# Optimization experiments

Hardware: AMD Instinct MI355X
Metric: run time of the kernel (lower is better)

The kernel has to match this reference:

```python
import jax, jax.numpy as jnp
import numpy as np

NEG_INF = -1e9

def setup_inputs() -> dict:
    key = jax.random.key(0)
    ks = jax.random.split(key, 8)
    B, Np1, D, k = 16, 10001, 128, 16
    return {
        "query": jax.random.normal(ks[0], (B, D), jnp.float32),
        "psi_prime": jax.random.normal(ks[1], (B, Np1, D), jnp.float32),
        "knn_indices": jax.random.randint(ks[2], (B, Np1, k), 0, Np1, jnp.int64),
        "mask": jnp.zeros((B, Np1), dtype=bool),
        "current_coords": jax.random.uniform(ks[3], (B, 2), jnp.float32),
        "all_coords": jax.random.uniform(ks[4], (B, Np1, 2), jnp.float32),
        "demands": jax.random.uniform(ks[5], (B, Np1), jnp.float32),
        "lambda_param": jnp.float32(0.1),
        "mu_param": jnp.float32(0.5),
        "nu_param": jnp.float32(0.0),
    }

def _eknn(psi_prime, knn_indices):
    # psi_prime: [B, N+1, D], knn_indices: [B, N+1, k] -> interference [B, N+1]
    B, Np1, k = knn_indices.shape
    D = psi_prime.shape[-1]
    flat_idx = knn_indices.reshape(B, Np1 * k, 1)  # gather along node axis
    neighbors = jnp.take_along_axis(psi_prime, flat_idx, axis=1).reshape(B, Np1, k, D)
    return jnp.einsum("bnd,bnkd->bn", psi_prime, neighbors)

def reference(query, psi_prime, knn_indices, mask, current_coords, all_coords,
              demands, lambda_param, mu_param, nu_param):
    capacity = 1.0  # default forward arg
    context_scores = jnp.einsum("bnd,bd->bn", psi_prime, query)
    interference = _eknn(psi_prime, knn_indices)
    dist_to_nodes = jnp.linalg.norm(all_coords - current_coords[:, None, :], axis=-1)
    mu_eff = jnp.clip(mu_param, 0.0, 20.0)
    lam_eff = jnp.clip(lambda_param, -2.0, 3.0)
    nu_eff = jnp.clip(nu_param, -2.0, 3.0)
    scores = context_scores + lam_eff * interference - mu_eff * dist_to_nodes
    cap_val = max(float(capacity), 1e-8)
    scores = scores + nu_eff * (demands / cap_val)
    scores = jnp.where(mask, NEG_INF, scores)
    return jax.nn.log_softmax(scores, axis=-1)
```

## Files before the change

### kernel.cpp

```cpp
#include <hip/hip_runtime.h>
#include <math.h>

#define BATCH 16
#define NP1   10001
#define KNN   16
#define DIM   128
#define NEG_INF_F (-1e9f)
#define TOTAL_NODES ((long)BATCH * NP1)
#define SLAB_BYTES  ((size_t)BATCH * NP1 * DIM)
#define NXCD 8
#define EXP_OFF 60.0f
#define NBUCK 64

template <int SEL>
__device__ inline float f8tof(unsigned u) {
#if __has_builtin(__builtin_amdgcn_cvt_f32_fp8)
    return __builtin_amdgcn_cvt_f32_fp8((int)u, SEL);
#else
    const unsigned x = (u >> (8 * SEL)) & 0xFFu;
    const unsigned bits = ((x & 0x80u) << 24) | (((x & 0x7Fu) << 20) + 0x3C000000u);
    return (x & 0x7Fu) ? __uint_as_float(bits) : 0.f;
#endif
}

#if !__has_builtin(__builtin_amdgcn_cvt_pk_fp8_f32)
__device__ inline unsigned enc1_fp8(float f) {
    const unsigned u = __float_as_uint(f);
    const unsigned s = (u >> 31) << 7;
    unsigned v = u + 0x80000u;
    int e8 = (int)((v >> 23) & 0xFFu) - 120;
    if (e8 <= 0) return s;
    if (e8 > 15) { e8 = 15; v |= 0x700000u; }
    return s | ((unsigned)e8 << 3) | ((v >> 20) & 7u);
}
#endif

__device__ inline unsigned pk_fp8x4(float4 v) {
#if __has_builtin(__builtin_amdgcn_cvt_pk_fp8_f32)
    int w = __builtin_amdgcn_cvt_pk_fp8_f32(v.x, v.y, 0, false);
    w = __builtin_amdgcn_cvt_pk_fp8_f32(v.z, v.w, w, true);
    return (unsigned)w;
#else
    return enc1_fp8(v.x) | (enc1_fp8(v.y) << 8) | (enc1_fp8(v.z) << 16) | (enc1_fp8(v.w) << 24);
#endif
}

__device__ inline unsigned xcd_chunk_swizzle(unsigned b, unsigned nwg) {
    const unsigned xcd = b % NXCD, i = b / NXCD;
    const unsigned q = nwg / NXCD, r = nwg % NXCD;
    const unsigned base = (xcd < r) ? xcd * (q + 1) : r * (q + 1) + (xcd - r) * q;
    return base + i;
}

__global__ __launch_bounds__(256) void hs_prep_kernel(
    const float* __restrict__ query,
    const float* __restrict__ psi,
    const float* __restrict__ cur,
    const float* __restrict__ coords,
    const float* __restrict__ demands,
    const float* __restrict__ mu_p,
    const float* __restrict__ nu_p,
    unsigned* __restrict__ slab,
    float* __restrict__ out,
    float* __restrict__ bucket)
{
    if (blockIdx.x == 0) {
#pragma unroll
        for (int i = 0; i < (BATCH * NBUCK) / 256; ++i)
            bucket[threadIdx.x + i * 256] = 0.f;
    }

    const unsigned lb = xcd_chunk_swizzle(blockIdx.x, gridDim.x);
    const long row = (long)lb * 8 + (threadIdx.x >> 5);
    if (row >= TOTAL_NODES) return;
    const int l32 = threadIdx.x & 31;
    const int b = (int)(row / NP1);

    const float4 v = ((const float4*)psi)[row * 32 + l32];
    const float4 q = ((const float4*)query)[(long)b * 32 + l32];

    slab[row * 32 + l32] = pk_fp8x4(v);

    float ctx = v.x * q.x + v.y * q.y + v.z * q.z + v.w * q.w;
#pragma unroll
    for (int off = 16; off > 0; off >>= 1) ctx += __shfl_xor(ctx, off, 64);

    if (l32 == 0) {
        const float mu = fminf(fmaxf(mu_p[0], 0.f), 20.f);
        const float nu = fminf(fmaxf(nu_p[0], -2.f), 3.f);
        const float dx = coords[row * 2 + 0] - cur[b * 2 + 0];
        const float dy = coords[row * 2 + 1] - cur[b * 2 + 1];
        out[row] = ctx - mu * sqrtf(dx * dx + dy * dy) + nu * demands[row];
    }
}

__global__ __launch_bounds__(256) void hs_gather_kernel(
    const int* __restrict__ knn,
    const unsigned char* __restrict__ mask,
    const uint2* __restrict__ slab2,
    const float* __restrict__ lam_p,
    float* __restrict__ out,
    float* __restrict__ bucket)
{
    __shared__ float s_val[16];
    __shared__ int   s_bat[16];

    const unsigned lb = xcd_chunk_swizzle(blockIdx.x, gridDim.x);
    const int wid  = threadIdx.x >> 6;
    const int lane = threadIdx.x & 63;
    const int qw   = lane >> 4;
    const int l16  = lane & 15;
    const long node = ((long)lb * 4 + wid) * 4 + qw;
    const int b = (int)(node / NP1);
    const uint2* gb = slab2 + (long)b * NP1 * 16;

    float base = 0.f; int mk = 0;
    if (l16 == 0) { base = out[node]; mk = mask[node]; }

    const uint2 p = slab2[node * 16 + l16];
    const float pf0 = f8tof<0>(p.x), pf1 = f8tof<1>(p.x), pf2 = f8tof<2>(p.x), pf3 = f8tof<3>(p.x);
    const float pf4 = f8tof<0>(p.y), pf5 = f8tof<1>(p.y), pf6 = f8tof<2>(p.y), pf7 = f8tof<3>(p.y);

    const int4* kp = (const int4*)(knn + node * KNN);
    const int4 k0 = kp[0], k1 = kp[1], k2 = kp[2], k3 = kp[3];

    uint2 nb[KNN];
    nb[ 0] = gb[(long)k0.x * 16 + l16];
    nb[ 1] = gb[(long)k0.y * 16 + l16];
    nb[ 2] = gb[(long)k0.z * 16 + l16];
    nb[ 3] = gb[(long)k0.w * 16 + l16];
    nb[ 4] = gb[(long)k1.x * 16 + l16];
    nb[ 5] = gb[(long)k1.y * 16 + l16];
    nb[ 6] = gb[(long)k1.z * 16 + l16];
    nb[ 7] = gb[(long)k1.w * 16 + l16];
    nb[ 8] = gb[(long)k2.x * 16 + l16];
    nb[ 9] = gb[(long)k2.y * 16 + l16];
    nb[10] = gb[(long)k2.z * 16 + l16];
    nb[11] = gb[(long)k2.w * 16 + l16];
    nb[12] = gb[(long)k3.x * 16 + l16];
    nb[13] = gb[(long)k3.y * 16 + l16];
    nb[14] = gb[(long)k3.z * 16 + l16];
    nb[15] = gb[(long)k3.w * 16 + l16];

    float a0 = 0.f, a1 = 0.f, a2 = 0.f, a3 = 0.f;
    float a4 = 0.f, a5 = 0.f, a6 = 0.f, a7 = 0.f;
#pragma unroll
    for (int t = 0; t < KNN; ++t) {
        a0 = fmaf(f8tof<0>(nb[t].x), pf0, a0);
        a1 = fmaf(f8tof<1>(nb[t].x), pf1, a1);
        a2 = fmaf(f8tof<2>(nb[t].x), pf2, a2);
        a3 = fmaf(f8tof<3>(nb[t].x), pf3, a3);
        a4 = fmaf(f8tof<0>(nb[t].y), pf4, a4);
        a5 = fmaf(f8tof<1>(nb[t].y), pf5, a5);
        a6 = fmaf(f8tof<2>(nb[t].y), pf6, a6);
        a7 = fmaf(f8tof<3>(nb[t].y), pf7, a7);
    }
    float interf = ((a0 + a1) + (a2 + a3)) + ((a4 + a5) + (a6 + a7));

#pragma unroll
    for (int off = 8; off > 0; off >>= 1) interf += __shfl_xor(interf, off, 64);

    const int slot = wid * 4 + qw;
    if (l16 == 0) {
        const float lam = fminf(fmaxf(lam_p[0], -2.f), 3.f);
        float s = base + lam * interf;
        if (mk) s = NEG_INF_F;
        out[node] = s;
        s_val[slot] = expf(s - EXP_OFF);
        s_bat[slot] = b;
    }
    __syncthreads();

    if (threadIdx.x == 0) {
        float sum0 = 0.f, sum1 = 0.f;
        const int b0 = s_bat[0];
        int b1 = -1;
#pragma unroll
        for (int i = 0; i < 16; ++i) {
            if (s_bat[i] == b0) sum0 += s_val[i];
            else { b1 = s_bat[i]; sum1 += s_val[i]; }
        }
        const int bk = blockIdx.x & (NBUCK - 1);
        atomicAdd(&bucket[b0 * NBUCK + bk], sum0);
        if (b1 >= 0) atomicAdd(&bucket[b1 * NBUCK + bk], sum1);
    }
}

__global__ __launch_bounds__(256) void hs_finalize_kernel(
    float* __restrict__ out, const float* __restrict__ bucket)
{
    __shared__ float s_part[256];
    __shared__ float s_lse[BATCH];

    {
        const int t = threadIdx.x;
        const int bb = t >> 4, j = t & 15;
        s_part[t] = bucket[bb * NBUCK + j] + bucket[bb * NBUCK + j + 16]
                  + bucket[bb * NBUCK + j + 32] + bucket[bb * NBUCK + j + 48];
    }
    __syncthreads();
    if (threadIdx.x < BATCH) {
        float s = 0.f;
#pragma unroll
        for (int i = 0; i < 16; ++i) s += s_part[threadIdx.x * 16 + i];
        s_lse[threadIdx.x] = EXP_OFF + logf(s);
    }
    __syncthreads();

    const long t = (long)blockIdx.x * blockDim.x + threadIdx.x;
    const long n4 = TOTAL_NODES / 4;
    if (t >= n4) return;
    float4 v = ((float4*)out)[t];
    const long e0 = t * 4;
    v.x -= s_lse[(int)((e0    ) / NP1)];
    v.y -= s_lse[(int)((e0 + 1) / NP1)];
    v.z -= s_lse[(int)((e0 + 2) / NP1)];
    v.w -= s_lse[(int)((e0 + 3) / NP1)];
    ((float4*)out)[t] = v;
}

__global__ __launch_bounds__(256) void hs_scores_f32_kernel(
    const float* __restrict__ query, const float* __restrict__ psi,
    const int* __restrict__ knn, const unsigned char* __restrict__ mask,
    const float* __restrict__ cur, const float* __restrict__ coords,
    const float* __restrict__ demands, const float* __restrict__ lam_p,
    const float* __restrict__ mu_p, const float* __restrict__ nu_p,
    float* __restrict__ out)
{
    const int wid  = threadIdx.x >> 6;
    const int lane = threadIdx.x & 63;
    const int half = lane >> 5;
    const int l32  = lane & 31;
    const long node = (long)blockIdx.x * 4 + wid;
    if (node >= TOTAL_NODES) return;
    const int b = (int)(node / NP1);

    const float4* psi4 = (const float4*)psi;
    const float4* gb   = psi4 + (long)b * NP1 * 32;

    const float4 p = psi4[node * 32 + l32];
    const float4 q = ((const float4*)query)[(long)b * 32 + l32];
    float ctx = p.x * q.x + p.y * q.y + p.z * q.z + p.w * q.w;

    const int2* kp2 = (const int2*)(knn + node * KNN);
    int idxs[KNN / 2];
#pragma unroll
    for (int t = 0; t < KNN / 2; ++t) {
        const int2 pr = kp2[t];
        idxs[t] = half ? pr.y : pr.x;
    }
    float4 nb[KNN / 2];
#pragma unroll
    for (int t = 0; t < KNN / 2; ++t) nb[t] = gb[(long)idxs[t] * 32 + l32];

    float4 s0;
    s0.x = ((nb[0].x + nb[1].x) + (nb[2].x + nb[3].x)) + ((nb[4].x + nb[5].x) + (nb[6].x + nb[7].x));
    s0.y = ((nb[0].y + nb[1].y) + (nb[2].y + nb[3].y)) + ((nb[4].y + nb[5].y) + (nb[6].y + nb[7].y));
    s0.z = ((nb[0].z + nb[1].z) + (nb[2].z + nb[3].z)) + ((nb[4].z + nb[5].z) + (nb[6].z + nb[7].z));
    s0.w = ((nb[0].w + nb[1].w) + (nb[2].w + nb[3].w)) + ((nb[4].w + nb[5].w) + (nb[6].w + nb[7].w));
    float interf = p.x * s0.x + p.y * s0.y + p.z * s0.z + p.w * s0.w;

#pragma unroll
    for (int off = 32; off > 0; off >>= 1) {
        ctx    += __shfl_xor(ctx, off, 64);
        interf += __shfl_xor(interf, off, 64);
    }
    if (lane == 0) {
        const float lam = fminf(fmaxf(lam_p[0], -2.f), 3.f);
        const float mu  = fminf(fmaxf(mu_p[0],   0.f), 20.f);
        const float nu  = fminf(fmaxf(nu_p[0],  -2.f), 3.f);
        const float dx = coords[node * 2 + 0] - cur[b * 2 + 0];
        const float dy = coords[node * 2 + 1] - cur[b * 2 + 1];
        float s = 0.5f * ctx + lam * interf - mu * sqrtf(dx * dx + dy * dy) + nu * demands[node];
        if (mask[node]) s = NEG_INF_F;
        out[node] = s;
    }
}

#define LSM_T 1024
__global__ __launch_bounds__(LSM_T) void hs_lsm_kernel(float* __restrict__ out)
{
    const int b = blockIdx.x;
    float* row = out + (long)b * NP1;
    const int lane = threadIdx.x & 63;
    const int wid  = threadIdx.x >> 6;
    __shared__ float red[LSM_T / 64];

    float v[10];
    float mx = -INFINITY;
#pragma unroll
    for (int i = 0; i < 10; ++i) {
        const int idx = threadIdx.x + i * LSM_T;
        v[i] = (idx < NP1) ? row[idx] : -INFINITY;
        mx = fmaxf(mx, v[i]);
    }
#pragma unroll
    for (int off = 32; off > 0; off >>= 1) mx = fmaxf(mx, __shfl_xor(mx, off, 64));
    if (lane == 0) red[wid] = mx;
    __syncthreads();
    if (wid == 0) {
        float m = (lane < LSM_T / 64) ? red[lane] : -INFINITY;
#pragma unroll
        for (int off = 8; off > 0; off >>= 1) m = fmaxf(m, __shfl_xor(m, off, 64));
        if (lane == 0) red[0] = m;
    }
    __syncthreads();
    mx = red[0];
    __syncthreads();

    float sum = 0.f;
#pragma unroll
    for (int i = 0; i < 10; ++i) {
        const int idx = threadIdx.x + i * LSM_T;
        if (idx < NP1) sum += expf(v[i] - mx);
    }
#pragma unroll
    for (int off = 32; off > 0; off >>= 1) sum += __shfl_xor(sum, off, 64);
    if (lane == 0) red[wid] = sum;
    __syncthreads();
    if (wid == 0) {
        float s = (lane < LSM_T / 64) ? red[lane] : 0.f;
#pragma unroll
        for (int off = 8; off > 0; off >>= 1) s += __shfl_xor(s, off, 64);
        if (lane == 0) red[0] = s;
    }
    __syncthreads();
    const float lse = mx + logf(red[0]);
#pragma unroll
    for (int i = 0; i < 10; ++i) {
        const int idx = threadIdx.x + i * LSM_T;
        if (idx < NP1) row[idx] = v[i] - lse;
    }
}

extern "C" void kernel_launch(void* const* d_in, const int* in_sizes, int n_in,
                              void* d_out, int out_size, void* d_ws, size_t ws_size,
                              hipStream_t stream) {
    (void)in_sizes; (void)n_in; (void)out_size;

    const float* query   = (const float*)d_in[0];
    const float* psi     = (const float*)d_in[1];
    const int*   knn     = (const int*)d_in[2];
    const unsigned char* mask = (const unsigned char*)d_in[3];
    const float* cur     = (const float*)d_in[4];
    const float* coords  = (const float*)d_in[5];
    const float* demands = (const float*)d_in[6];
    const float* lam_p   = (const float*)d_in[7];
    const float* mu_p    = (const float*)d_in[8];
    const float* nu_p    = (const float*)d_in[9];
    float* out = (float*)d_out;

    const size_t bucket_bytes = (size_t)BATCH * NBUCK * sizeof(float);

    if (ws_size >= SLAB_BYTES + bucket_bytes) {
        unsigned* slab = (unsigned*)d_ws;
        float* bucket  = (float*)((char*)d_ws + SLAB_BYTES);

        const int prep_blocks = (int)((TOTAL_NODES + 7) / 8);
        hipLaunchKernelGGL(hs_prep_kernel, dim3(prep_blocks), dim3(256), 0, stream,
                           query, psi, cur, coords, demands, mu_p, nu_p, slab, out,
                           bucket);

        const int gat_blocks = (int)(TOTAL_NODES / 16);
        hipLaunchKernelGGL(hs_gather_kernel, dim3(gat_blocks), dim3(256), 0, stream,
                           knn, mask, (const uint2*)d_ws, lam_p, out, bucket);

        const int fin_blocks = (int)((TOTAL_NODES / 4 + 255) / 256);
        hipLaunchKernelGGL(hs_finalize_kernel, dim3(fin_blocks), dim3(256), 0, stream,
                           out, bucket);
    } else {
        const int blocks = (int)((TOTAL_NODES + 3) / 4);
        hipLaunchKernelGGL(hs_scores_f32_kernel, dim3(blocks), dim3(256), 0, stream,
                           query, psi, knn, mask, cur, coords, demands,
                           lam_p, mu_p, nu_p, out);
        hipLaunchKernelGGL(hs_lsm_kernel, dim3(BATCH), dim3(LSM_T), 0, stream, out);
    }
}
```

Measured before the change: 58.98 us.

## Fuse prep, gather and finalize into one cooperative producer/consumer kernel

Replaces the three-kernel chain with a single cooperative launch. 512 producer blocks quantize psi to fp8 and compute base scores batch by batch, then publish per-batch ready flags. 512 consumer blocks spin on those flags and run the kNN gather as soon as their batch is ready, and a grid sync precedes the log-softmax normalization. The aim is to overlap the prep and gather phases and remove launch gaps. In exchange it adds flag polling, a memset, per-launch host queries, a grid barrier, and a fixed grid that may underuse the device. The f32 fallback path is removed, so too small a workspace now produces no output.

```diff
diff --git a/kernel.cpp b/kernel.cpp
--- a/kernel.cpp
+++ b/kernel.cpp
@@ -1,5 +1,8 @@
 #include <hip/hip_runtime.h>
+#include <hip/hip_cooperative_groups.h>
 #include <math.h>
+
+namespace cg = cooperative_groups;
 
 #define BATCH 16
 #define NP1   10001
@@ -8,9 +11,15 @@
 #define NEG_INF_F (-1e9f)
 #define TOTAL_NODES ((long)BATCH * NP1)
 #define SLAB_BYTES  ((size_t)BATCH * NP1 * DIM)
-#define NXCD 8
 #define EXP_OFF 60.0f
 #define NBUCK 64
+
+#define PROD_BLOCKS 512
+#define CONS_BLOCKS 512
+#define FUSE_GRID   (PROD_BLOCKS + CONS_BLOCKS)
+#define NGRP_PREP   ((NP1 + 7) / 8)
+#define NGRP_GAT    ((int)(TOTAL_NODES / 16))
+#define FLAG_STRIDE 32
 
 template <int SEL>
 __device__ inline float f8tof(unsigned u) {
@@ -45,6 +54,7 @@
 #endif
 }
 
+#define NXCD 8
 __device__ inline unsigned xcd_chunk_swizzle(unsigned b, unsigned nwg) {
     const unsigned xcd = b % NXCD, i = b / NXCD;
     const unsigned q = nwg / NXCD, r = nwg % NXCD;
@@ -52,39 +62,200 @@
     return base + i;
 }
 
-__global__ __launch_bounds__(256) void hs_prep_kernel(
-    const float* __restrict__ query,
-    const float* __restrict__ psi,
-    const float* __restrict__ cur,
-    const float* __restrict__ coords,
-    const float* __restrict__ demands,
-    const float* __restrict__ mu_p,
-    const float* __restrict__ nu_p,
+__global__ __launch_bounds__(256, 4) void hs_fused_kernel(
+    const float* __restrict__ query, const float* __restrict__ psi,
+    const int* __restrict__ knn, const unsigned char* __restrict__ mask,
+    const float* __restrict__ cur, const float* __restrict__ coords,
+    const float* __restrict__ demands, const float* __restrict__ lam_p,
+    const float* __restrict__ mu_p, const float* __restrict__ nu_p,
     unsigned* __restrict__ slab,
     float* __restrict__ out,
-    float* __restrict__ bucket)
+    float* __restrict__ bucket,
+    unsigned* __restrict__ flags)
+{
+    __shared__ float s_val[16];
+    __shared__ int   s_bat[16];
+    __shared__ float s_part[256];
+    __shared__ float s_lse[BATCH];
+
+    const int tid = threadIdx.x;
+
+    if (blockIdx.x < PROD_BLOCKS) {
+        const int l32 = tid & 31;
+        const int hw  = tid >> 5;
+        const float mu = fminf(fmaxf(mu_p[0], 0.f), 20.f);
+        const float nuv = fminf(fmaxf(nu_p[0], -2.f), 3.f);
+        for (int b = 0; b < BATCH; ++b) {
+            const float4 q = ((const float4*)query)[b * 32 + l32];
+            const float cx = cur[2 * b], cy = cur[2 * b + 1];
+            const long rb = (long)b * NP1;
+            for (int g = blockIdx.x; g < NGRP_PREP; g += PROD_BLOCKS) {
+                const int r = g * 8 + hw;
+                if (r < NP1) {
+                    const long row = rb + r;
+                    const float4 v = ((const float4*)psi)[row * 32 + l32];
+                    slab[row * 32 + l32] = pk_fp8x4(v);
+                    float ctx = v.x * q.x + v.y * q.y + v.z * q.z + v.w * q.w;
+#pragma unroll
+                    for (int off = 16; off > 0; off >>= 1) ctx += __shfl_xor(ctx, off, 64);
+                    if (l32 == 0) {
+                        const float dx = coords[row * 2] - cx, dy = coords[row * 2 + 1] - cy;
+                        out[row] = ctx - mu * sqrtf(dx * dx + dy * dy) + nuv * demands[row];
+                    }
+                }
+            }
+            __threadfence();
+            __syncthreads();
+            if (tid == 0) atomicAdd(&flags[b * FLAG_STRIDE], 1u);
+        }
+    } else {
+        const int cblk = blockIdx.x - PROD_BLOCKS;
+        const int wid = tid >> 6, lane = tid & 63;
+        const int qw = lane >> 4, l16 = lane & 15;
+        const float lam = fminf(fmaxf(lam_p[0], -2.f), 3.f);
+        int b_ready = -1;
+        for (int vg = cblk; vg < NGRP_GAT; vg += CONS_BLOCKS) {
+            const long node0 = (long)vg * 16;
+            const int b_hi = (int)((node0 + 15) / NP1);
+            if (b_hi > b_ready) {
+                if (tid == 0) {
+                    while (__hip_atomic_load(&flags[b_hi * FLAG_STRIDE],
+                                             __ATOMIC_ACQUIRE, __HIP_MEMORY_SCOPE_AGENT)
+                           < (unsigned)PROD_BLOCKS)
+                        __builtin_amdgcn_s_sleep(16);
+                }
+                __syncthreads();
+                __threadfence();
+                b_ready = b_hi;
+            }
+            const long node = node0 + wid * 4 + qw;
+            const int b = (int)(node / NP1);
+            const uint2* gb = (const uint2*)slab + (long)b * NP1 * 16;
+
+            float base = 0.f; int mk = 0;
+            if (l16 == 0) { base = out[node]; mk = mask[node]; }
+
+            const uint2 p = ((const uint2*)slab)[node * 16 + l16];
+            const float pf0 = f8tof<0>(p.x), pf1 = f8tof<1>(p.x), pf2 = f8tof<2>(p.x), pf3 = f8tof<3>(p.x);
+            const float pf4 = f8tof<0>(p.y), pf5 = f8tof<1>(p.y), pf6 = f8tof<2>(p.y), pf7 = f8tof<3>(p.y);
+
+            const int4* kp = (const int4*)(knn + node * KNN);
+            const int4 k0 = kp[0], k1 = kp[1], k2 = kp[2], k3 = kp[3];
+
+            uint2 nb[KNN];
+            nb[ 0] = gb[(long)k0.x * 16 + l16];
+            nb[ 1] = gb[(long)k0.y * 16 + l16];
+            nb[ 2] = gb[(long)k0.z * 16 + l16];
+            nb[ 3] = gb[(long)k0.w * 16 + l16];
+            nb[ 4] = gb[(long)k1.x * 16 + l16];
+            nb[ 5] = gb[(long)k1.y * 16 + l16];
+            nb[ 6] = gb[(long)k1.z * 16 + l16];
+            nb[ 7] = gb[(long)k1.w * 16 + l16];
+            nb[ 8] = gb[(long)k2.x * 16 + l16];
+            nb[ 9] = gb[(long)k2.y * 16 + l16];
+            nb[10] = gb[(long)k2.z * 16 + l16];
+            nb[11] = gb[(long)k2.w * 16 + l16];
+            nb[12] = gb[(long)k3.x * 16 + l16];
+            nb[13] = gb[(long)k3.y * 16 + l16];
+            nb[14] = gb[(long)k3.z * 16 + l16];
+            nb[15] = gb[(long)k3.w * 16 + l16];
+
+            float a0 = 0.f, a1 = 0.f, a2 = 0.f, a3 = 0.f;
+            float a4 = 0.f, a5 = 0.f, a6 = 0.f, a7 = 0.f;
+#pragma unroll
+            for (int t = 0; t < KNN; ++t) {
+                a0 = fmaf(f8tof<0>(nb[t].x), pf0, a0);
+                a1 = fmaf(f8tof<1>(nb[t].x), pf1, a1);
+                a2 = fmaf(f8tof<2>(nb[t].x), pf2, a2);
+                a3 = fmaf(f8tof<3>(nb[t].x), pf3, a3);
+                a4 = fmaf(f8tof<0>(nb[t].y), pf4, a4);
+                a5 = fmaf(f8tof<1>(nb[t].y), pf5, a5);
+                a6 = fmaf(f8tof<2>(nb[t].y), pf6, a6);
+                a7 = fmaf(f8tof<3>(nb[t].y), pf7, a7);
+            }
+            float interf = ((a0 + a1) + (a2 + a3)) + ((a4 + a5) + (a6 + a7));
+#pragma unroll
+            for (int off = 8; off > 0; off >>= 1) interf += __shfl_xor(interf, off, 64);
+
+            const int slot = wid * 4 + qw;
+            if (l16 == 0) {
+                float s = base + lam * interf;
+                if (mk) s = NEG_INF_F;
+                out[node] = s;
+                s_val[slot] = expf(s - EXP_OFF);
+                s_bat[slot] = b;
+            }
+            __syncthreads();
+            if (tid == 0) {
+                float sum0 = 0.f, sum1 = 0.f;
+                const int b0 = s_bat[0];
+                int b1 = -1;
+#pragma unroll
+                for (int i = 0; i < 16; ++i) {
+                    if (s_bat[i] == b0) sum0 += s_val[i];
+                    else { b1 = s_bat[i]; sum1 += s_val[i]; }
+                }
+                const int bk = vg & (NBUCK - 1);
+                atomicAdd(&bucket[b0 * NBUCK + bk], sum0);
+                if (b1 >= 0) atomicAdd(&bucket[b1 * NBUCK + bk], sum1);
+            }
+            __syncthreads();
+        }
+    }
+
+    __threadfence();
+    cg::this_grid().sync();
+    __threadfence();
+
+    {
+        const int t = tid;
+        const int bb = t >> 4, j = t & 15;
+        s_part[t] = bucket[bb * NBUCK + j] + bucket[bb * NBUCK + j + 16]
+                  + bucket[bb * NBUCK + j + 32] + bucket[bb * NBUCK + j + 48];
+        __syncthreads();
+        if (t < BATCH) {
+            float s = 0.f;
+#pragma unroll
+            for (int i = 0; i < 16; ++i) s += s_part[t * 16 + i];
+            s_lse[t] = EXP_OFF + logf(s);
+        }
+        __syncthreads();
+        const long n4 = TOTAL_NODES / 4;
+        for (long i = (long)blockIdx.x * 256 + t; i < n4; i += (long)FUSE_GRID * 256) {
+            float4 v = ((float4*)out)[i];
+            const long e0 = i * 4;
+            v.x -= s_lse[(int)((e0    ) / NP1)];
+            v.y -= s_lse[(int)((e0 + 1) / NP1)];
+            v.z -= s_lse[(int)((e0 + 2) / NP1)];
+            v.w -= s_lse[(int)((e0 + 3) / NP1)];
+            ((float4*)out)[i] = v;
+        }
+    }
+}
+
+__global__ __launch_bounds__(256) void hs_prep_kernel(
+    const float* __restrict__ query, const float* __restrict__ psi,
+    const float* __restrict__ cur, const float* __restrict__ coords,
+    const float* __restrict__ demands, const float* __restrict__ mu_p,
+    const float* __restrict__ nu_p, unsigned* __restrict__ slab,
+    float* __restrict__ out, float* __restrict__ bucket)
 {
     if (blockIdx.x == 0) {
 #pragma unroll
         for (int i = 0; i < (BATCH * NBUCK) / 256; ++i)
             bucket[threadIdx.x + i * 256] = 0.f;
     }
-
     const unsigned lb = xcd_chunk_swizzle(blockIdx.x, gridDim.x);
     const long row = (long)lb * 8 + (threadIdx.x >> 5);
     if (row >= TOTAL_NODES) return;
     const int l32 = threadIdx.x & 31;
     const int b = (int)(row / NP1);
-
     const float4 v = ((const float4*)psi)[row * 32 + l32];
     const float4 q = ((const float4*)query)[(long)b * 32 + l32];
-
     slab[row * 32 + l32] = pk_fp8x4(v);
-
     float ctx = v.x * q.x + v.y * q.y + v.z * q.z + v.w * q.w;
 #pragma unroll
     for (int off = 16; off > 0; off >>= 1) ctx += __shfl_xor(ctx, off, 64);
-
     if (l32 == 0) {
         const float mu = fminf(fmaxf(mu_p[0], 0.f), 20.f);
         const float nu = fminf(fmaxf(nu_p[0], -2.f), 3.f);
@@ -95,55 +266,35 @@
 }
 
 __global__ __launch_bounds__(256) void hs_gather_kernel(
-    const int* __restrict__ knn,
-    const unsigned char* __restrict__ mask,
-    const uint2* __restrict__ slab2,
-    const float* __restrict__ lam_p,
-    float* __restrict__ out,
-    float* __restrict__ bucket)
+    const int* __restrict__ knn, const unsigned char* __restrict__ mask,
+    const uint2* __restrict__ slab2, const float* __restrict__ lam_p,
+    float* __restrict__ out, float* __restrict__ bucket)
 {
     __shared__ float s_val[16];
     __shared__ int   s_bat[16];
-
     const unsigned lb = xcd_chunk_swizzle(blockIdx.x, gridDim.x);
-    const int wid  = threadIdx.x >> 6;
-    const int lane = threadIdx.x & 63;
-    const int qw   = lane >> 4;
-    const int l16  = lane & 15;
+    const int wid = threadIdx.x >> 6, lane = threadIdx.x & 63;
+    const int qw = lane >> 4, l16 = lane & 15;
     const long node = ((long)lb * 4 + wid) * 4 + qw;
     const int b = (int)(node / NP1);
     const uint2* gb = slab2 + (long)b * NP1 * 16;
-
     float base = 0.f; int mk = 0;
     if (l16 == 0) { base = out[node]; mk = mask[node]; }
-
     const uint2 p = slab2[node * 16 + l16];
     const float pf0 = f8tof<0>(p.x), pf1 = f8tof<1>(p.x), pf2 = f8tof<2>(p.x), pf3 = f8tof<3>(p.x);
     const float pf4 = f8tof<0>(p.y), pf5 = f8tof<1>(p.y), pf6 = f8tof<2>(p.y), pf7 = f8tof<3>(p.y);
-
     const int4* kp = (const int4*)(knn + node * KNN);
     const int4 k0 = kp[0], k1 = kp[1], k2 = kp[2], k3 = kp[3];
-
     uint2 nb[KNN];
-    nb[ 0] = gb[(long)k0.x * 16 + l16];
-    nb[ 1] = gb[(long)k0.y * 16 + l16];
-    nb[ 2] = gb[(long)k0.z * 16 + l16];
-    nb[ 3] = gb[(long)k0.w * 16 + l16];
-    nb[ 4] = gb[(long)k1.x * 16 + l16];
-    nb[ 5] = gb[(long)k1.y * 16 + l16];
-    nb[ 6] = gb[(long)k1.z * 16 + l16];
-    nb[ 7] = gb[(long)k1.w * 16 + l16];
-    nb[ 8] = gb[(long)k2.x * 16 + l16];
-    nb[ 9] = gb[(long)k2.y * 16 + l16];
-    nb[10] = gb[(long)k2.z * 16 + l16];
-    nb[11] = gb[(long)k2.w * 16 + l16];
-    nb[12] = gb[(long)k3.x * 16 + l16];
-    nb[13] = gb[(long)k3.y * 16 + l16];
-    nb[14] = gb[(long)k3.z * 16 + l16];
-    nb[15] = gb[(long)k3.w * 16 + l16];
-
-    float a0 = 0.f, a1 = 0.f, a2 = 0.f, a3 = 0.f;
-    float a4 = 0.f, a5 = 0.f, a6 = 0.f, a7 = 0.f;
+    nb[ 0] = gb[(long)k0.x * 16 + l16]; nb[ 1] = gb[(long)k0.y * 16 + l16];
+    nb[ 2] = gb[(long)k0.z * 16 + l16]; nb[ 3] = gb[(long)k0.w * 16 + l16];
+    nb[ 4] = gb[(long)k1.x * 16 + l16]; nb[ 5] = gb[(long)k1.y * 16 + l16];
+    nb[ 6] = gb[(long)k1.z * 16 + l16]; nb[ 7] = gb[(long)k1.w * 16 + l16];
+    nb[ 8] = gb[(long)k2.x * 16 + l16]; nb[ 9] = gb[(long)k2.y * 16 + l16];
+    nb[10] = gb[(long)k2.z * 16 + l16]; nb[11] = gb[(long)k2.w * 16 + l16];
+    nb[12] = gb[(long)k3.x * 16 + l16]; nb[13] = gb[(long)k3.y * 16 + l16];
+    nb[14] = gb[(long)k3.z * 16 + l16]; nb[15] = gb[(long)k3.w * 16 + l16];
+    float a0 = 0.f, a1 = 0.f, a2 = 0.f, a3 = 0.f, a4 = 0.f, a5 = 0.f, a6 = 0.f, a7 = 0.f;
 #pragma unroll
     for (int t = 0; t < KNN; ++t) {
         a0 = fmaf(f8tof<0>(nb[t].x), pf0, a0);
@@ -156,10 +307,8 @@
         a7 = fmaf(f8tof<3>(nb[t].y), pf7, a7);
     }
     float interf = ((a0 + a1) + (a2 + a3)) + ((a4 + a5) + (a6 + a7));
-
 #pragma unroll
     for (int off = 8; off > 0; off >>= 1) interf += __shfl_xor(interf, off, 64);
-
     const int slot = wid * 4 + qw;
     if (l16 == 0) {
         const float lam = fminf(fmaxf(lam_p[0], -2.f), 3.f);
@@ -170,7 +319,6 @@
         s_bat[slot] = b;
     }
     __syncthreads();
-
     if (threadIdx.x == 0) {
         float sum0 = 0.f, sum1 = 0.f;
         const int b0 = s_bat[0];
@@ -191,7 +339,6 @@
 {
     __shared__ float s_part[256];
     __shared__ float s_lse[BATCH];
-
     {
         const int t = threadIdx.x;
         const int bb = t >> 4, j = t & 15;
@@ -206,7 +353,6 @@
         s_lse[threadIdx.x] = EXP_OFF + logf(s);
     }
     __syncthreads();
-
     const long t = (long)blockIdx.x * blockDim.x + threadIdx.x;
     const long n4 = TOTAL_NODES / 4;
     if (t >= n4) return;
@@ -217,120 +363,6 @@
     v.z -= s_lse[(int)((e0 + 2) / NP1)];
     v.w -= s_lse[(int)((e0 + 3) / NP1)];
     ((float4*)out)[t] = v;
-}
-
-__global__ __launch_bounds__(256) void hs_scores_f32_kernel(
-    const float* __restrict__ query, const float* __restrict__ psi,
-    const int* __restrict__ knn, const unsigned char* __restrict__ mask,
-    const float* __restrict__ cur, const float* __restrict__ coords,
-    const float* __restrict__ demands, const float* __restrict__ lam_p,
-    const float* __restrict__ mu_p, const float* __restrict__ nu_p,
-    float* __restrict__ out)
-{
-    const int wid  = threadIdx.x >> 6;
-    const int lane = threadIdx.x & 63;
-    const int half = lane >> 5;
-    const int l32  = lane & 31;
-    const long node = (long)blockIdx.x * 4 + wid;
-    if (node >= TOTAL_NODES) return;
-    const int b = (int)(node / NP1);
-
-    const float4* psi4 = (const float4*)psi;
-    const float4* gb   = psi4 + (long)b * NP1 * 32;
-
-    const float4 p = psi4[node * 32 + l32];
-    const float4 q = ((const float4*)query)[(long)b * 32 + l32];
-    float ctx = p.x * q.x + p.y * q.y + p.z * q.z + p.w * q.w;
-
-    const int2* kp2 = (const int2*)(knn + node * KNN);
-    int idxs[KNN / 2];
-#pragma unroll
-    for (int t = 0; t < KNN / 2; ++t) {
-        const int2 pr = kp2[t];
-        idxs[t] = half ? pr.y : pr.x;
-    }
-    float4 nb[KNN / 2];
-#pragma unroll
-    for (int t = 0; t < KNN / 2; ++t) nb[t] = gb[(long)idxs[t] * 32 + l32];
-
-    float4 s0;
-    s0.x = ((nb[0].x + nb[1].x) + (nb[2].x + nb[3].x)) + ((nb[4].x + nb[5].x) + (nb[6].x + nb[7].x));
-    s0.y = ((nb[0].y + nb[1].y) + (nb[2].y + nb[3].y)) + ((nb[4].y + nb[5].y) + (nb[6].y + nb[7].y));
-    s0.z = ((nb[0].z + nb[1].z) + (nb[2].z + nb[3].z)) + ((nb[4].z + nb[5].z) + (nb[6].z + nb[7].z));
-    s0.w = ((nb[0].w + nb[1].w) + (nb[2].w + nb[3].w)) + ((nb[4].w + nb[5].w) + (nb[6].w + nb[7].w));
-    float interf = p.x * s0.x + p.y * s0.y + p.z * s0.z + p.w * s0.w;
-
-#pragma unroll
-    for (int off = 32; off > 0; off >>= 1) {
-        ctx    += __shfl_xor(ctx, off, 64);
-        interf += __shfl_xor(interf, off, 64);
-    }
-    if (lane == 0) {
-        const float lam = fminf(fmaxf(lam_p[0], -2.f), 3.f);
-        const float mu  = fminf(fmaxf(mu_p[0],   0.f), 20.f);
-        const float nu  = fminf(fmaxf(nu_p[0],  -2.f), 3.f);
-        const float dx = coords[node * 2 + 0] - cur[b * 2 + 0];
-        const float dy = coords[node * 2 + 1] - cur[b * 2 + 1];
-        float s = 0.5f * ctx + lam * interf - mu * sqrtf(dx * dx + dy * dy) + nu * demands[node];
-        if (mask[node]) s = NEG_INF_F;
-        out[node] = s;
-    }
-}
-
-#define LSM_T 1024
-__global__ __launch_bounds__(LSM_T) void hs_lsm_kernel(float* __restrict__ out)
-{
-    const int b = blockIdx.x;
-    float* row = out + (long)b * NP1;
-    const int lane = threadIdx.x & 63;
-    const int wid  = threadIdx.x >> 6;
-    __shared__ float red[LSM_T / 64];
-
-    float v[10];
-    float mx = -INFINITY;
-#pragma unroll
-    for (int i = 0; i < 10; ++i) {
-        const int idx = threadIdx.x + i * LSM_T;
-        v[i] = (idx < NP1) ? row[idx] : -INFINITY;
-        mx = fmaxf(mx, v[i]);
-    }
-#pragma unroll
-    for (int off = 32; off > 0; off >>= 1) mx = fmaxf(mx, __shfl_xor(mx, off, 64));
-    if (lane == 0) red[wid] = mx;
-    __syncthreads();
-    if (wid == 0) {
-        float m = (lane < LSM_T / 64) ? red[lane] : -INFINITY;
-#pragma unroll
-        for (int off = 8; off > 0; off >>= 1) m = fmaxf(m, __shfl_xor(m, off, 64));
-        if (lane == 0) red[0] = m;
-    }
-    __syncthreads();
-    mx = red[0];
-    __syncthreads();
-
-    float sum = 0.f;
-#pragma unroll
-    for (int i = 0; i < 10; ++i) {
-        const int idx = threadIdx.x + i * LSM_T;
-        if (idx < NP1) sum += expf(v[i] - mx);
-    }
-#pragma unroll
-    for (int off = 32; off > 0; off >>= 1) sum += __shfl_xor(sum, off, 64);
-    if (lane == 0) red[wid] = sum;
-    __syncthreads();
-    if (wid == 0) {
-        float s = (lane < LSM_T / 64) ? red[lane] : 0.f;
-#pragma unroll
-        for (int off = 8; off > 0; off >>= 1) s += __shfl_xor(s, off, 64);
-        if (lane == 0) red[0] = s;
-    }
-    __syncthreads();
-    const float lse = mx + logf(red[0]);
-#pragma unroll
-    for (int i = 0; i < 10; ++i) {
-        const int idx = threadIdx.x + i * LSM_T;
-        if (idx < NP1) row[idx] = v[i] - lse;
-    }
 }
 
 extern "C" void kernel_launch(void* const* d_in, const int* in_sizes, int n_in,
@@ -351,28 +383,42 @@
     float* out = (float*)d_out;
 
     const size_t bucket_bytes = (size_t)BATCH * NBUCK * sizeof(float);
-
-    if (ws_size >= SLAB_BYTES + bucket_bytes) {
-        unsigned* slab = (unsigned*)d_ws;
-        float* bucket  = (float*)((char*)d_ws + SLAB_BYTES);
+    const size_t flags_bytes  = (size_t)BATCH * FLAG_STRIDE * sizeof(unsigned);
+    const size_t need = SLAB_BYTES + bucket_bytes + flags_bytes;
+
+    int dev = 0;
+    hipGetDevice(&dev);
+    int coop = 0;
+    hipDeviceGetAttribute(&coop, hipDeviceAttributeCooperativeLaunch, dev);
+    int maxb = 0;
+    hipOccupancyMaxActiveBlocksPerMultiprocessor(&maxb, (const void*)hs_fused_kernel, 256, 0);
+
+    if (ws_size >= need && coop && maxb >= 4) {
+        unsigned* slab   = (unsigned*)d_ws;
+        float*    bucket = (float*)((char*)d_ws + SLAB_BYTES);
+        unsigned* flags  = (unsigned*)((char*)d_ws + SLAB_BYTES + bucket_bytes);
+
+        hipMemsetAsync(bucket, 0, bucket_bytes + flags_bytes, stream);
+
+        void* kargs[] = {
+            (void*)&query, (void*)&psi, (void*)&knn, (void*)&mask, (void*)&cur,
+            (void*)&coords, (void*)&demands, (void*)&lam_p, (void*)&mu_p, (void*)&nu_p,
+            (void*)&slab, (void*)&out, (void*)&bucket, (void*)&flags
+        };
+        hipLaunchCooperativeKernel((const void*)hs_fused_kernel,
+                                   dim3(FUSE_GRID), dim3(256), kargs, 0, stream);
+    } else if (ws_size >= need) {
+        unsigned* slab   = (unsigned*)d_ws;
+        float*    bucket = (float*)((char*)d_ws + SLAB_BYTES);
 
         const int prep_blocks = (int)((TOTAL_NODES + 7) / 8);
         hipLaunchKernelGGL(hs_prep_kernel, dim3(prep_blocks), dim3(256), 0, stream,
-                           query, psi, cur, coords, demands, mu_p, nu_p, slab, out,
-                           bucket);
-
+                           query, psi, cur, coords, demands, mu_p, nu_p, slab, out, bucket);
         const int gat_blocks = (int)(TOTAL_NODES / 16);
         hipLaunchKernelGGL(hs_gather_kernel, dim3(gat_blocks), dim3(256), 0, stream,
                            knn, mask, (const uint2*)d_ws, lam_p, out, bucket);
-
         const int fin_blocks = (int)((TOTAL_NODES / 4 + 255) / 256);
         hipLaunchKernelGGL(hs_finalize_kernel, dim3(fin_blocks), dim3(256), 0, stream,
                            out, bucket);
-    } else {
-        const int blocks = (int)((TOTAL_NODES + 3) / 4);
-        hipLaunchKernelGGL(hs_scores_f32_kernel, dim3(blocks), dim3(256), 0, stream,
-                           query, psi, knn, mask, cur, coords, demands,
-                           lam_p, mu_p, nu_p, out);
-        hipLaunchKernelGGL(hs_lsm_kernel, dim3(BATCH), dim3(LSM_T), 0, stream, out);
-    }
-}
+    }
+}
```

Result: no change. 59.20 us (+0.4%).
